# Optimization experiments

Hardware: AMD Instinct MI355X
Metric: run time of the kernel (lower is better)

Reference implementation:

```python
import jax, jax.numpy as jnp
import numpy as np

BN_EPS = 1e-5


def _batchnorm(h, gamma, beta):
    # training-mode BatchNorm1d: batch mean, biased variance
    mean = jnp.mean(h, axis=0)
    var = jnp.mean((h - mean) ** 2, axis=0)
    return (h - mean) * jax.lax.rsqrt(var + BN_EPS) * gamma + beta


def setup_inputs() -> dict:
    key = jax.random.key(0)
    ks = jax.random.split(key, 6)
    N, E = 50000, 800000
    atom, nbr = 128, 64
    d_in = 2 * atom + nbr          # 320
    d_out = 2 * atom               # 256
    x = jax.random.normal(ks[0], (N, atom), dtype=jnp.float32)
    edge_index = jax.random.randint(ks[1], (2, E), 0, N, dtype=jnp.int64)
    edge_attr = jax.random.normal(ks[2], (E, nbr), dtype=jnp.float32)
    W = jax.random.normal(ks[3], (d_in, d_out), dtype=jnp.float32) / np.sqrt(d_in)
    b = jax.random.normal(ks[4], (d_out,), dtype=jnp.float32) * 0.01
    gamma1 = jnp.ones((d_out,), dtype=jnp.float32)
    beta1 = jnp.zeros((d_out,), dtype=jnp.float32)
    gamma2 = jnp.ones((atom,), dtype=jnp.float32)
    beta2 = jnp.zeros((atom,), dtype=jnp.float32)
    return {"x": x, "edge_index": edge_index, "edge_attr": edge_attr,
            "W": W, "b": b, "gamma1": gamma1, "beta1": beta1,
            "gamma2": gamma2, "beta2": beta2}


def reference(x, edge_index, edge_attr, W, b, gamma1, beta1, gamma2, beta2):
    N, atom = x.shape
    src = edge_index[0]  # destination of scatter-sum (as in source)
    dst = edge_index[1]
    xi = x[src]                                   # [E, atom]
    xj = x[dst]                                   # [E, atom]
    total = jnp.concatenate([xi, xj, edge_attr], axis=-1)   # [E, 2*atom+nbr]
    gated = total @ W + b                         # [E, 2*atom]
    gated = _batchnorm(gated, gamma1, beta1)
    nbr_filter, nbr_core = jnp.split(gated, 2, axis=-1)
    msg = jax.nn.sigmoid(nbr_filter) * jax.nn.softplus(nbr_core)  # [E, atom]
    summed = jax.ops.segment_sum(msg, src, num_segments=N)        # [N, atom]
    return _batchnorm(summed, gamma2, beta2)
```

## Files before the change

kernel.cpp:

```cpp
#include <hip/hip_runtime.h>
#include <hip/hip_bf16.h>
#include <math.h>

#define BN_EPS 1e-5f

typedef __bf16 bf8 __attribute__((ext_vector_type(8)));
typedef unsigned short us8 __attribute__((ext_vector_type(8)));
typedef float f32x4 __attribute__((ext_vector_type(4)));

static __device__ __forceinline__ unsigned short f2bf(float f) {
  unsigned int u = __float_as_uint(f);
  unsigned int r = (u + 0x7FFFu + ((u >> 16) & 1u)) >> 16;
  return (unsigned short)r;
}
static __device__ __forceinline__ float bf2f(unsigned short v) {
  return __uint_as_float(((unsigned int)v) << 16);
}
static __device__ __forceinline__ float sigmoidf_(float x) {
  return 1.0f / (1.0f + __expf(-x));
}
static __device__ __forceinline__ float softplusf_(float x) {
  return fmaxf(x, 0.0f) + log1pf(__expf(-fabsf(x)));
}


__global__ void k_zero(int* __restrict__ deg, float* __restrict__ stats, int N) {
  int stride = gridDim.x * blockDim.x;
  int i = blockIdx.x * blockDim.x + threadIdx.x;
  for (int j = i; j < N; j += stride) deg[j] = 0;
  for (int j = i; j < 768; j += stride) stats[j] = 0.f;
}

__global__ void k_deg(const int* __restrict__ ei, int* __restrict__ deg, int E) {
  int e = blockIdx.x * blockDim.x + threadIdx.x;
  if (e < E) atomicAdd(&deg[ei[e]], 1);
}

__global__ __launch_bounds__(1024) void k_scan(const int* __restrict__ deg,
                                               int* __restrict__ offs,
                                               int* __restrict__ cursor, int N) {
  __shared__ int wsum[16];
  __shared__ int carry_s;
  int tid = threadIdx.x;
  int lane = tid & 63, wv = tid >> 6;
  if (tid == 0) carry_s = 0;
  __syncthreads();
  for (int base = 0; base < N; base += 1024) {
    int i = base + tid;
    int v = (i < N) ? deg[i] : 0;
    int x = v;
    #pragma unroll
    for (int off = 1; off < 64; off <<= 1) {
      int t = __shfl_up(x, off, 64);
      if (lane >= off) x += t;
    }
    if (lane == 63) wsum[wv] = x;
    __syncthreads();
    if (wv == 0 && lane < 16) {
      int y = wsum[lane];
      #pragma unroll
      for (int off = 1; off < 16; off <<= 1) {
        int t = __shfl_up(y, off, 64);
        if (lane >= off) y += t;
      }
      wsum[lane] = y;
    }
    __syncthreads();
    int woff = (wv == 0) ? 0 : wsum[wv - 1];
    int carry = carry_s;
    int incl = woff + x;
    if (i < N) { int o = carry + incl - v; offs[i] = o; cursor[i] = o; }
    __syncthreads();
    if (tid == 1023) carry_s = carry + incl;
    __syncthreads();
  }
}

__global__ __launch_bounds__(256) void k_wt(const float* __restrict__ W,
                                            unsigned short* __restrict__ WT) {
  int idx = blockIdx.x * 256 + threadIdx.x;
  int k = idx >> 8, c = idx & 255;
  WT[c * 320 + k] = f2bf(W[idx]);
}

__global__ __launch_bounds__(256, 3) void k_gemm1(
    const float* __restrict__ x, const int* __restrict__ ei,
    const float* __restrict__ ea, const unsigned short* __restrict__ WT,
    const float* __restrict__ bias, unsigned short* __restrict__ gated,
    int* __restrict__ cursor, int E) {
  __shared__ unsigned short F[64][328];
  __shared__ int ssrc[64], sdst[64], spos[64];
  int tid = threadIdx.x;
  int e0 = blockIdx.x * 64;
  if (tid < 64) {
    int e = e0 + tid;
    int s = 0, d = 0, p = 0;
    if (e < E) {
      s = ei[e]; d = ei[E + e];
      p = atomicAdd(&cursor[s], 1);
    }
    ssrc[tid] = s; sdst[tid] = d; spos[tid] = p;
  }
  __syncthreads();

  {
    int q = tid & 31, r2 = tid >> 5;
    #pragma unroll
    for (int it = 0; it < 8; ++it) {
      int r = r2 + it * 8;
      float4 v = *(const float4*)(x + (size_t)ssrc[r] * 128 + q * 4);
      ushort4 h = {f2bf(v.x), f2bf(v.y), f2bf(v.z), f2bf(v.w)};
      *(ushort4*)&F[r][q * 4] = h;
    }
    #pragma unroll
    for (int it = 0; it < 8; ++it) {
      int r = r2 + it * 8;
      float4 v = *(const float4*)(x + (size_t)sdst[r] * 128 + q * 4);
      ushort4 h = {f2bf(v.x), f2bf(v.y), f2bf(v.z), f2bf(v.w)};
      *(ushort4*)&F[r][128 + q * 4] = h;
    }
    int q2 = tid & 15, r4 = tid >> 4;
    #pragma unroll
    for (int it = 0; it < 4; ++it) {
      int r = r4 + it * 16;
      int e = e0 + r;
      float4 v = make_float4(0.f, 0.f, 0.f, 0.f);
      if (e < E) v = *(const float4*)(ea + (size_t)e * 64 + q2 * 4);
      ushort4 h = {f2bf(v.x), f2bf(v.y), f2bf(v.z), f2bf(v.w)};
      *(ushort4*)&F[r][256 + q2 * 4] = h;
    }
  }
  __syncthreads();

  int w = tid >> 6, l = tid & 63;
  int l15 = l & 15, lg = l >> 4;
  f32x4 acc[4][4] = {};
  const unsigned short* wtb = WT + (size_t)((w * 4) * 16 + l15) * 320 + lg * 8;
  #pragma unroll 1
  for (int k0 = 0; k0 < 10; ++k0) {
    bf8 bfr[4];
    #pragma unroll
    for (int nt = 0; nt < 4; ++nt) {
      us8 raw = *(const us8*)&F[nt * 16 + l15][k0 * 32 + lg * 8];
      bfr[nt] = __builtin_bit_cast(bf8, raw);
    }
    #pragma unroll
    for (int ctl = 0; ctl < 4; ++ctl) {
      us8 araw = *(const us8*)(wtb + (size_t)ctl * (16 * 320) + k0 * 32);
      bf8 afr = __builtin_bit_cast(bf8, araw);
      #pragma unroll
      for (int nt = 0; nt < 4; ++nt)
        acc[ctl][nt] = __builtin_amdgcn_mfma_f32_16x16x32_bf16(afr, bfr[nt], acc[ctl][nt], 0, 0, 0);
    }
  }

  #pragma unroll
  for (int ctl = 0; ctl < 4; ++ctl) {
    int col0 = (w * 4 + ctl) * 16 + lg * 4;
    float4 bv = *(const float4*)(bias + col0);
    #pragma unroll
    for (int nt = 0; nt < 4; ++nt) {
      int el = nt * 16 + l15;
      if (e0 + el < E) {
        f32x4 a = acc[ctl][nt];
        ushort4 hv = {f2bf(a[0] + bv.x), f2bf(a[1] + bv.y),
                      f2bf(a[2] + bv.z), f2bf(a[3] + bv.w)};
        *(ushort4*)(gated + (size_t)spos[el] * 256 + col0) = hv;
      }
    }
  }
}

__global__ __launch_bounds__(256) void k_bn1stats(const unsigned short* __restrict__ gated,
                                                  float* __restrict__ stats, int E) {
  __shared__ float s_[256], q_[256];
  int tid = threadIdx.x;
  s_[tid] = 0.f; q_[tid] = 0.f;
  __syncthreads();
  int w = tid >> 6, l = tid & 63;
  int c0 = l * 4;
  float s0 = 0, s1 = 0, s2 = 0, s3 = 0, q0 = 0, q1 = 0, q2 = 0, q3 = 0;
  for (int r = blockIdx.x * 4 + w; r < E; r += gridDim.x * 4) {
    ushort4 raw = *(const ushort4*)(gated + (size_t)r * 256 + c0);
    float v0 = bf2f(raw.x), v1 = bf2f(raw.y), v2 = bf2f(raw.z), v3 = bf2f(raw.w);
    s0 += v0; q0 += v0 * v0;
    s1 += v1; q1 += v1 * v1;
    s2 += v2; q2 += v2 * v2;
    s3 += v3; q3 += v3 * v3;
  }
  atomicAdd(&s_[c0], s0);     atomicAdd(&q_[c0], q0);
  atomicAdd(&s_[c0 + 1], s1); atomicAdd(&q_[c0 + 1], q1);
  atomicAdd(&s_[c0 + 2], s2); atomicAdd(&q_[c0 + 2], q2);
  atomicAdd(&s_[c0 + 3], s3); atomicAdd(&q_[c0 + 3], q3);
  __syncthreads();
  atomicAdd(&stats[tid], s_[tid]);
  atomicAdd(&stats[256 + tid], q_[tid]);
}

__global__ void k_bn1fin(float* __restrict__ stats, const float* __restrict__ g1,
                         const float* __restrict__ b1, float Einv) {
  int j = threadIdx.x;
  float mu = stats[j] * Einv;
  float var = stats[256 + j] * Einv - mu * mu;
  float s = g1[j] * rsqrtf(var + BN_EPS);
  stats[768 + j] = s;
  stats[1024 + j] = b1[j] - mu * s;
}

__global__ __launch_bounds__(256) void k_phase2(
    const unsigned short* __restrict__ gated,
    const int* __restrict__ offs, const int* __restrict__ deg,
    const float* __restrict__ stats, float* __restrict__ out, int N) {
  int wid = (blockIdx.x * 256 + threadIdx.x) >> 6;
  int lane = threadIdx.x & 63;
  if (wid >= N) return;
  const float* scale1 = stats + 768;
  const float* shift1 = stats + 1024;
  int c0 = lane * 2;
  float sf0 = scale1[c0], sf1 = scale1[c0 + 1];
  float hf0 = shift1[c0], hf1 = shift1[c0 + 1];
  float sc0 = scale1[128 + c0], sc1 = scale1[128 + c0 + 1];
  float hc0 = shift1[128 + c0], hc1 = shift1[128 + c0 + 1];
  int st = offs[wid], d = deg[wid];
  const unsigned short* rowp = gated + (size_t)st * 256;
  float a0 = 0.f, a1 = 0.f;
  for (int i = 0; i < d; ++i) {
    unsigned int fw = *(const unsigned int*)(rowp + c0);
    unsigned int cw = *(const unsigned int*)(rowp + 128 + c0);
    float f0 = bf2f((unsigned short)(fw & 0xFFFFu)) * sf0 + hf0;
    float f1 = bf2f((unsigned short)(fw >> 16)) * sf1 + hf1;
    float q0 = bf2f((unsigned short)(cw & 0xFFFFu)) * sc0 + hc0;
    float q1 = bf2f((unsigned short)(cw >> 16)) * sc1 + hc1;
    a0 += sigmoidf_(f0) * softplusf_(q0);
    a1 += sigmoidf_(f1) * softplusf_(q1);
    rowp += 256;
  }
  *(float2*)(out + (size_t)wid * 128 + c0) = make_float2(a0, a1);
}

__global__ __launch_bounds__(256) void k_bn2stats(const float* __restrict__ out,
                                                  float* __restrict__ stats, int N) {
  float* sum2 = stats + 512;
  float* sq2 = stats + 640;
  __shared__ float s_[128], q_[128];
  int c = threadIdx.x & 127, h = threadIdx.x >> 7;
  float s = 0.f, q = 0.f;
  for (int r = blockIdx.x * 2 + h; r < N; r += gridDim.x * 2) {
    float v = out[(size_t)r * 128 + c];
    s += v; q += v * v;
  }
  if (h == 0) { s_[c] = s; q_[c] = q; }
  __syncthreads();
  if (h == 1) { s_[c] += s; q_[c] += q; }
  __syncthreads();
  if (h == 0) { atomicAdd(&sum2[c], s_[c]); atomicAdd(&sq2[c], q_[c]); }
}

__global__ __launch_bounds__(256) void k_bn2norm(float* __restrict__ out,
                                                 const float* __restrict__ stats,
                                                 const float* __restrict__ g2,
                                                 const float* __restrict__ b2, int N) {
  const float* sum2 = stats + 512;
  const float* sq2 = stats + 640;
  float Ninv = 1.0f / (float)N;
  size_t total = (size_t)N * 32;
  for (size_t i = (size_t)blockIdx.x * blockDim.x + threadIdx.x; i < total;
       i += (size_t)gridDim.x * blockDim.x) {
    float4 v = *((const float4*)out + i);
    int c = (int)((i & 31) << 2);
    float r[4] = {v.x, v.y, v.z, v.w};
    #pragma unroll
    for (int j = 0; j < 4; ++j) {
      float mu = sum2[c + j] * Ninv;
      float var = sq2[c + j] * Ninv - mu * mu;
      float sc = g2[c + j] * rsqrtf(var + BN_EPS);
      r[j] = (r[j] - mu) * sc + b2[c + j];
    }
    *((float4*)out + i) = make_float4(r[0], r[1], r[2], r[3]);
  }
}

extern "C" void kernel_launch(void* const* d_in, const int* in_sizes, int n_in,
                              void* d_out, int out_size, void* d_ws, size_t ws_size,
                              hipStream_t stream) {
  (void)n_in; (void)out_size;
  const float* x  = (const float*)d_in[0];
  const int*   ei = (const int*)d_in[1];
  const float* ea = (const float*)d_in[2];
  const float* W  = (const float*)d_in[3];
  const float* b  = (const float*)d_in[4];
  const float* g1 = (const float*)d_in[5];
  const float* b1 = (const float*)d_in[6];
  const float* g2 = (const float*)d_in[7];
  const float* b2 = (const float*)d_in[8];
  int N = in_sizes[0] / 128;
  int E = in_sizes[1] / 2;
  float* out = (float*)d_out;

  char* base = (char*)d_ws;
  size_t off = 0;
  auto take = [&](size_t bytes) {
    size_t o = off;
    off = (off + bytes + 255) & ~(size_t)255;
    return o;
  };
  size_t oWT     = take((size_t)256 * 320 * sizeof(unsigned short));
  size_t oGated  = take((size_t)E * 256 * sizeof(unsigned short));
  size_t oDeg    = take((size_t)N * sizeof(int));
  size_t oOffs   = take((size_t)N * sizeof(int));
  size_t oCur    = take((size_t)N * sizeof(int));
  size_t oStats  = take(2048 * sizeof(float));
  if (off > ws_size) return;

  unsigned short* WT = (unsigned short*)(base + oWT);
  unsigned short* gated = (unsigned short*)(base + oGated);
  int* deg = (int*)(base + oDeg);
  int* offs = (int*)(base + oOffs);
  int* cursor = (int*)(base + oCur);
  float* stats = (float*)(base + oStats);

  k_zero<<<256, 256, 0, stream>>>(deg, stats, N);
  k_deg<<<(E + 255) / 256, 256, 0, stream>>>(ei, deg, E);
  k_scan<<<1, 1024, 0, stream>>>(deg, offs, cursor, N);
  k_wt<<<320, 256, 0, stream>>>(W, WT);
  k_gemm1<<<(E + 63) / 64, 256, 0, stream>>>(x, ei, ea, WT, b, gated, cursor, E);
  k_bn1stats<<<1024, 256, 0, stream>>>(gated, stats, E);
  k_bn1fin<<<1, 256, 0, stream>>>(stats, g1, b1, 1.0f / (float)E);
  k_phase2<<<(N + 3) / 4, 256, 0, stream>>>(gated, offs, deg, stats, out, N);
  k_bn2stats<<<512, 256, 0, stream>>>(out, stats, N);
  k_bn2norm<<<1024, 256, 0, stream>>>(out, stats, g2, b2, N);
}
```

Baseline: 1.385 ms.

## Precompute per-node projections, shrink edge GEMM to edge_attr, fuse BN1 stats

The concat-GEMM is split algebraically. x@W[0:128] and x@W[128:256] are computed once per node into a bf16 table P. Each edge then gathers two P rows and adds a small K=64 MFMA GEMM over edge_attr. The bias is dropped because training-mode BatchNorm cancels it. BN1 sum and sum-of-squares are accumulated inside the persistent fused kernel, which removes the separate pass over the gated buffer. The degree count and scan kernels are also vectorized to int4. The cost is an extra N×512 bf16 workspace and an extra bf16 rounding of the node projections before summation.

```diff
diff --git a/kernel.cpp b/kernel.cpp
--- a/kernel.cpp
+++ b/kernel.cpp
@@ -32,8 +32,17 @@
 }
 
 __global__ void k_deg(const int* __restrict__ ei, int* __restrict__ deg, int E) {
-  int e = blockIdx.x * blockDim.x + threadIdx.x;
-  if (e < E) atomicAdd(&deg[ei[e]], 1);
+  int idx = blockIdx.x * 256 + threadIdx.x;
+  int e = idx * 4;
+  if (e + 3 < E) {
+    int4 v = *(const int4*)(ei + e);
+    atomicAdd(&deg[v.x], 1);
+    atomicAdd(&deg[v.y], 1);
+    atomicAdd(&deg[v.z], 1);
+    atomicAdd(&deg[v.w], 1);
+  } else if (e < E) {
+    for (int k = e; k < E && k < e + 4; ++k) atomicAdd(&deg[ei[k]], 1);
+  }
 }
 
 __global__ __launch_bounds__(1024) void k_scan(const int* __restrict__ deg,
@@ -45,10 +54,21 @@
   int lane = tid & 63, wv = tid >> 6;
   if (tid == 0) carry_s = 0;
   __syncthreads();
-  for (int base = 0; base < N; base += 1024) {
-    int i = base + tid;
-    int v = (i < N) ? deg[i] : 0;
-    int x = v;
+  int N4 = (N + 3) >> 2;
+  for (int b4 = 0; b4 < N4; b4 += 1024) {
+    int i4 = b4 + tid;
+    int4 v = make_int4(0, 0, 0, 0);
+    int base = i4 * 4;
+    if (i4 < N4) {
+      if (base + 3 < N) v = *(const int4*)(deg + base);
+      else {
+        v.x = deg[base];
+        if (base + 1 < N) v.y = deg[base + 1];
+        if (base + 2 < N) v.z = deg[base + 2];
+      }
+    }
+    int tsum = v.x + v.y + v.z + v.w;
+    int x = tsum;
     #pragma unroll
     for (int off = 1; off < 64; off <<= 1) {
       int t = __shfl_up(x, off, 64);
@@ -66,135 +86,200 @@
       wsum[lane] = y;
     }
     __syncthreads();
-    int woff = (wv == 0) ? 0 : wsum[wv - 1];
     int carry = carry_s;
-    int incl = woff + x;
-    if (i < N) { int o = carry + incl - v; offs[i] = o; cursor[i] = o; }
-    __syncthreads();
-    if (tid == 1023) carry_s = carry + incl;
+    int pre = carry + ((wv == 0) ? 0 : wsum[wv - 1]) + (x - tsum);
+    if (i4 < N4) {
+      int o0 = pre, o1 = o0 + v.x, o2 = o1 + v.y, o3 = o2 + v.z;
+      if (base + 3 < N) {
+        *(int4*)(offs + base) = make_int4(o0, o1, o2, o3);
+        *(int4*)(cursor + base) = make_int4(o0, o1, o2, o3);
+      } else {
+        offs[base] = o0; cursor[base] = o0;
+        if (base + 1 < N) { offs[base + 1] = o1; cursor[base + 1] = o1; }
+        if (base + 2 < N) { offs[base + 2] = o2; cursor[base + 2] = o2; }
+      }
+    }
+    __syncthreads();
+    if (tid == 1023) carry_s = carry + wsum[15];
     __syncthreads();
   }
 }
 
 __global__ __launch_bounds__(256) void k_wt(const float* __restrict__ W,
-                                            unsigned short* __restrict__ WT) {
+                                            unsigned short* __restrict__ WT12,
+                                            unsigned short* __restrict__ W3T) {
   int idx = blockIdx.x * 256 + threadIdx.x;
-  int k = idx >> 8, c = idx & 255;
-  WT[c * 320 + k] = f2bf(W[idx]);
-}
-
-__global__ __launch_bounds__(256, 3) void k_gemm1(
-    const float* __restrict__ x, const int* __restrict__ ei,
-    const float* __restrict__ ea, const unsigned short* __restrict__ WT,
-    const float* __restrict__ bias, unsigned short* __restrict__ gated,
-    int* __restrict__ cursor, int E) {
-  __shared__ unsigned short F[64][328];
+  if (idx < 65536) {
+    int cc = idx >> 7, k = idx & 127;
+    int row = (cc < 256) ? k : (k + 128);
+    WT12[cc * 128 + k] = f2bf(W[(size_t)row * 256 + (cc & 255)]);
+  } else {
+    int j = idx - 65536;
+    int c = j >> 6, k = j & 63;
+    W3T[c * 64 + k] = f2bf(W[(size_t)(256 + k) * 256 + c]);
+  }
+}
+
+__global__ __launch_bounds__(256) void k_pgemm(const float* __restrict__ x,
+                                               const unsigned short* __restrict__ WT12,
+                                               unsigned short* __restrict__ P, int N) {
+  __shared__ unsigned short xs[64][136];
+  int row0 = blockIdx.x * 64;
+  int half = blockIdx.y;
+  int tid = threadIdx.x;
+  for (int i = tid; i < 2048; i += 256) {
+    int r = i >> 5, c4 = (i & 31) * 4;
+    int gr = row0 + r;
+    float4 v = make_float4(0.f, 0.f, 0.f, 0.f);
+    if (gr < N) v = *(const float4*)(x + (size_t)gr * 128 + c4);
+    ushort4 h = {f2bf(v.x), f2bf(v.y), f2bf(v.z), f2bf(v.w)};
+    *(ushort4*)&xs[r][c4] = h;
+  }
+  __syncthreads();
+  int w = tid >> 6, l = tid & 63, l15 = l & 15, lg = l >> 4;
+  f32x4 acc[4][4] = {};
+  const unsigned short* wtb = WT12 + (size_t)(half * 256 + w * 64 + l15) * 128 + lg * 8;
+  #pragma unroll
+  for (int k0 = 0; k0 < 4; ++k0) {
+    bf8 bfr[4];
+    #pragma unroll
+    for (int nt = 0; nt < 4; ++nt) {
+      us8 raw = *(const us8*)&xs[nt * 16 + l15][k0 * 32 + lg * 8];
+      bfr[nt] = __builtin_bit_cast(bf8, raw);
+    }
+    #pragma unroll
+    for (int ctl = 0; ctl < 4; ++ctl) {
+      us8 araw = *(const us8*)(wtb + (size_t)ctl * (16 * 128) + k0 * 32);
+      bf8 afr = __builtin_bit_cast(bf8, araw);
+      #pragma unroll
+      for (int nt = 0; nt < 4; ++nt)
+        acc[ctl][nt] = __builtin_amdgcn_mfma_f32_16x16x32_bf16(afr, bfr[nt], acc[ctl][nt], 0, 0, 0);
+    }
+  }
+  #pragma unroll
+  for (int ctl = 0; ctl < 4; ++ctl) {
+    int pcol = half * 256 + w * 64 + ctl * 16 + lg * 4;
+    #pragma unroll
+    for (int nt = 0; nt < 4; ++nt) {
+      int prow = row0 + nt * 16 + l15;
+      if (prow < N) {
+        f32x4 a = acc[ctl][nt];
+        ushort4 hv = {f2bf(a[0]), f2bf(a[1]), f2bf(a[2]), f2bf(a[3])};
+        *(ushort4*)(P + (size_t)prow * 512 + pcol) = hv;
+      }
+    }
+  }
+}
+
+__global__ __launch_bounds__(256, 3) void k_fuse(
+    const int* __restrict__ ei, const float* __restrict__ ea,
+    const unsigned short* __restrict__ W3T, const unsigned short* __restrict__ P,
+    unsigned short* __restrict__ gated, int* __restrict__ cursor,
+    float* __restrict__ stats, int E, int ntiles) {
+  __shared__ unsigned short w3s[256][72];
+  __shared__ unsigned short eas[64][72];
   __shared__ int ssrc[64], sdst[64], spos[64];
   int tid = threadIdx.x;
-  int e0 = blockIdx.x * 64;
-  if (tid < 64) {
-    int e = e0 + tid;
-    int s = 0, d = 0, p = 0;
-    if (e < E) {
-      s = ei[e]; d = ei[E + e];
-      p = atomicAdd(&cursor[s], 1);
-    }
-    ssrc[tid] = s; sdst[tid] = d; spos[tid] = p;
-  }
-  __syncthreads();
-
-  {
-    int q = tid & 31, r2 = tid >> 5;
-    #pragma unroll
-    for (int it = 0; it < 8; ++it) {
-      int r = r2 + it * 8;
-      float4 v = *(const float4*)(x + (size_t)ssrc[r] * 128 + q * 4);
-      ushort4 h = {f2bf(v.x), f2bf(v.y), f2bf(v.z), f2bf(v.w)};
-      *(ushort4*)&F[r][q * 4] = h;
-    }
-    #pragma unroll
-    for (int it = 0; it < 8; ++it) {
-      int r = r2 + it * 8;
-      float4 v = *(const float4*)(x + (size_t)sdst[r] * 128 + q * 4);
-      ushort4 h = {f2bf(v.x), f2bf(v.y), f2bf(v.z), f2bf(v.w)};
-      *(ushort4*)&F[r][128 + q * 4] = h;
-    }
-    int q2 = tid & 15, r4 = tid >> 4;
-    #pragma unroll
-    for (int it = 0; it < 4; ++it) {
-      int r = r4 + it * 16;
+  int w = tid >> 6, l = tid & 63, l15 = l & 15, lg = l >> 4;
+
+  for (int i = tid; i < 2048; i += 256) {
+    int c = i >> 3, k8 = (i & 7) * 8;
+    *(us8*)&w3s[c][k8] = *(const us8*)(W3T + c * 64 + k8);
+  }
+
+  float sA[16] = {}, qA[16] = {};
+
+  for (int t = blockIdx.x; t < ntiles; t += gridDim.x) {
+    int e0 = t * 64;
+    __syncthreads();
+    if (tid < 64) {
+      int e = e0 + tid;
+      int s = 0, d = 0, p = 0;
+      if (e < E) {
+        s = ei[e]; d = ei[E + e];
+        p = atomicAdd(&cursor[s], 1);
+      }
+      ssrc[tid] = s; sdst[tid] = d; spos[tid] = p;
+    }
+    for (int i = tid; i < 1024; i += 256) {
+      int r = i >> 4, c4 = (i & 15) * 4;
       int e = e0 + r;
       float4 v = make_float4(0.f, 0.f, 0.f, 0.f);
-      if (e < E) v = *(const float4*)(ea + (size_t)e * 64 + q2 * 4);
+      if (e < E) v = *(const float4*)(ea + (size_t)e * 64 + c4);
       ushort4 h = {f2bf(v.x), f2bf(v.y), f2bf(v.z), f2bf(v.w)};
-      *(ushort4*)&F[r][256 + q2 * 4] = h;
-    }
-  }
-  __syncthreads();
-
-  int w = tid >> 6, l = tid & 63;
-  int l15 = l & 15, lg = l >> 4;
-  f32x4 acc[4][4] = {};
-  const unsigned short* wtb = WT + (size_t)((w * 4) * 16 + l15) * 320 + lg * 8;
-  #pragma unroll 1
-  for (int k0 = 0; k0 < 10; ++k0) {
-    bf8 bfr[4];
-    #pragma unroll
-    for (int nt = 0; nt < 4; ++nt) {
-      us8 raw = *(const us8*)&F[nt * 16 + l15][k0 * 32 + lg * 8];
-      bfr[nt] = __builtin_bit_cast(bf8, raw);
-    }
-    #pragma unroll
-    for (int ctl = 0; ctl < 4; ++ctl) {
-      us8 araw = *(const us8*)(wtb + (size_t)ctl * (16 * 320) + k0 * 32);
-      bf8 afr = __builtin_bit_cast(bf8, araw);
-      #pragma unroll
-      for (int nt = 0; nt < 4; ++nt)
-        acc[ctl][nt] = __builtin_amdgcn_mfma_f32_16x16x32_bf16(afr, bfr[nt], acc[ctl][nt], 0, 0, 0);
-    }
-  }
-
-  #pragma unroll
-  for (int ctl = 0; ctl < 4; ++ctl) {
-    int col0 = (w * 4 + ctl) * 16 + lg * 4;
-    float4 bv = *(const float4*)(bias + col0);
+      *(ushort4*)&eas[r][c4] = h;
+    }
+    __syncthreads();
+
+    f32x4 acc[4][4] = {};
+    #pragma unroll
+    for (int k0 = 0; k0 < 2; ++k0) {
+      bf8 bfr[4];
+      #pragma unroll
+      for (int nt = 0; nt < 4; ++nt) {
+        us8 raw = *(const us8*)&eas[nt * 16 + l15][k0 * 32 + lg * 8];
+        bfr[nt] = __builtin_bit_cast(bf8, raw);
+      }
+      #pragma unroll
+      for (int ctl = 0; ctl < 4; ++ctl) {
+        us8 araw = *(const us8*)&w3s[w * 64 + ctl * 16 + l15][k0 * 32 + lg * 8];
+        bf8 afr = __builtin_bit_cast(bf8, araw);
+        #pragma unroll
+        for (int nt = 0; nt < 4; ++nt)
+          acc[ctl][nt] = __builtin_amdgcn_mfma_f32_16x16x32_bf16(afr, bfr[nt], acc[ctl][nt], 0, 0, 0);
+      }
+    }
+
+    int sp_[4], sn_[4], dn_[4], ok_[4];
     #pragma unroll
     for (int nt = 0; nt < 4; ++nt) {
       int el = nt * 16 + l15;
-      if (e0 + el < E) {
+      sp_[nt] = spos[el]; sn_[nt] = ssrc[el]; dn_[nt] = sdst[el];
+      ok_[nt] = (e0 + el < E);
+    }
+    #pragma unroll
+    for (int ctl = 0; ctl < 4; ++ctl) {
+      int coff = w * 64 + ctl * 16 + lg * 4;
+      uint2 p1[4], p2[4];
+      #pragma unroll
+      for (int nt = 0; nt < 4; ++nt)
+        p1[nt] = *(const uint2*)(P + (size_t)sn_[nt] * 512 + coff);
+      #pragma unroll
+      for (int nt = 0; nt < 4; ++nt)
+        p2[nt] = *(const uint2*)(P + (size_t)dn_[nt] * 512 + 256 + coff);
+      #pragma unroll
+      for (int nt = 0; nt < 4; ++nt) {
         f32x4 a = acc[ctl][nt];
-        ushort4 hv = {f2bf(a[0] + bv.x), f2bf(a[1] + bv.y),
-                      f2bf(a[2] + bv.z), f2bf(a[3] + bv.w)};
-        *(ushort4*)(gated + (size_t)spos[el] * 256 + col0) = hv;
-      }
-    }
-  }
-}
-
-__global__ __launch_bounds__(256) void k_bn1stats(const unsigned short* __restrict__ gated,
-                                                  float* __restrict__ stats, int E) {
-  __shared__ float s_[256], q_[256];
-  int tid = threadIdx.x;
-  s_[tid] = 0.f; q_[tid] = 0.f;
-  __syncthreads();
-  int w = tid >> 6, l = tid & 63;
-  int c0 = l * 4;
-  float s0 = 0, s1 = 0, s2 = 0, s3 = 0, q0 = 0, q1 = 0, q2 = 0, q3 = 0;
-  for (int r = blockIdx.x * 4 + w; r < E; r += gridDim.x * 4) {
-    ushort4 raw = *(const ushort4*)(gated + (size_t)r * 256 + c0);
-    float v0 = bf2f(raw.x), v1 = bf2f(raw.y), v2 = bf2f(raw.z), v3 = bf2f(raw.w);
-    s0 += v0; q0 += v0 * v0;
-    s1 += v1; q1 += v1 * v1;
-    s2 += v2; q2 += v2 * v2;
-    s3 += v3; q3 += v3 * v3;
-  }
-  atomicAdd(&s_[c0], s0);     atomicAdd(&q_[c0], q0);
-  atomicAdd(&s_[c0 + 1], s1); atomicAdd(&q_[c0 + 1], q1);
-  atomicAdd(&s_[c0 + 2], s2); atomicAdd(&q_[c0 + 2], q2);
-  atomicAdd(&s_[c0 + 3], s3); atomicAdd(&q_[c0 + 3], q3);
-  __syncthreads();
-  atomicAdd(&stats[tid], s_[tid]);
-  atomicAdd(&stats[256 + tid], q_[tid]);
+        float g0 = a[0] + bf2f((unsigned short)(p1[nt].x & 0xFFFFu)) + bf2f((unsigned short)(p2[nt].x & 0xFFFFu));
+        float g1 = a[1] + bf2f((unsigned short)(p1[nt].x >> 16))     + bf2f((unsigned short)(p2[nt].x >> 16));
+        float g2 = a[2] + bf2f((unsigned short)(p1[nt].y & 0xFFFFu)) + bf2f((unsigned short)(p2[nt].y & 0xFFFFu));
+        float g3 = a[3] + bf2f((unsigned short)(p1[nt].y >> 16))     + bf2f((unsigned short)(p2[nt].y >> 16));
+        if (ok_[nt]) {
+          sA[ctl * 4 + 0] += g0; qA[ctl * 4 + 0] += g0 * g0;
+          sA[ctl * 4 + 1] += g1; qA[ctl * 4 + 1] += g1 * g1;
+          sA[ctl * 4 + 2] += g2; qA[ctl * 4 + 2] += g2 * g2;
+          sA[ctl * 4 + 3] += g3; qA[ctl * 4 + 3] += g3 * g3;
+          ushort4 hv = {f2bf(g0), f2bf(g1), f2bf(g2), f2bf(g3)};
+          *(ushort4*)(gated + (size_t)sp_[nt] * 256 + coff) = hv;
+        }
+      }
+    }
+  }
+
+  #pragma unroll
+  for (int i = 0; i < 16; ++i) {
+    float s = sA[i], q = qA[i];
+    #pragma unroll
+    for (int m = 1; m < 16; m <<= 1) {
+      s += __shfl_xor(s, m, 64);
+      q += __shfl_xor(q, m, 64);
+    }
+    if (l15 == 0) {
+      int col = w * 64 + (i >> 2) * 16 + lg * 4 + (i & 3);
+      atomicAdd(&stats[col], s);
+      atomicAdd(&stats[256 + col], q);
+    }
+  }
 }
 
 __global__ void k_bn1fin(float* __restrict__ stats, const float* __restrict__ g1,
@@ -288,7 +373,6 @@
   const int*   ei = (const int*)d_in[1];
   const float* ea = (const float*)d_in[2];
   const float* W  = (const float*)d_in[3];
-  const float* b  = (const float*)d_in[4];
   const float* g1 = (const float*)d_in[5];
   const float* b1 = (const float*)d_in[6];
   const float* g2 = (const float*)d_in[7];
@@ -304,7 +388,9 @@
     off = (off + bytes + 255) & ~(size_t)255;
     return o;
   };
-  size_t oWT     = take((size_t)256 * 320 * sizeof(unsigned short));
+  size_t oWT12   = take((size_t)512 * 128 * sizeof(unsigned short));
+  size_t oW3T    = take((size_t)256 * 64 * sizeof(unsigned short));
+  size_t oP      = take((size_t)N * 512 * sizeof(unsigned short));
   size_t oGated  = take((size_t)E * 256 * sizeof(unsigned short));
   size_t oDeg    = take((size_t)N * sizeof(int));
   size_t oOffs   = take((size_t)N * sizeof(int));
@@ -312,19 +398,22 @@
   size_t oStats  = take(2048 * sizeof(float));
   if (off > ws_size) return;
 
-  unsigned short* WT = (unsigned short*)(base + oWT);
+  unsigned short* WT12 = (unsigned short*)(base + oWT12);
+  unsigned short* W3T  = (unsigned short*)(base + oW3T);
+  unsigned short* P    = (unsigned short*)(base + oP);
   unsigned short* gated = (unsigned short*)(base + oGated);
   int* deg = (int*)(base + oDeg);
   int* offs = (int*)(base + oOffs);
   int* cursor = (int*)(base + oCur);
   float* stats = (float*)(base + oStats);
 
+  int ntiles = (E + 63) / 64;
   k_zero<<<256, 256, 0, stream>>>(deg, stats, N);
-  k_deg<<<(E + 255) / 256, 256, 0, stream>>>(ei, deg, E);
+  k_deg<<<(E / 4 + 255) / 256, 256, 0, stream>>>(ei, deg, E);
   k_scan<<<1, 1024, 0, stream>>>(deg, offs, cursor, N);
-  k_wt<<<320, 256, 0, stream>>>(W, WT);
-  k_gemm1<<<(E + 63) / 64, 256, 0, stream>>>(x, ei, ea, WT, b, gated, cursor, E);
-  k_bn1stats<<<1024, 256, 0, stream>>>(gated, stats, E);
+  k_wt<<<320, 256, 0, stream>>>(W, WT12, W3T);
+  k_pgemm<<<dim3((N + 63) / 64, 2), 256, 0, stream>>>(x, WT12, P, N);
+  k_fuse<<<2048, 256, 0, stream>>>(ei, ea, W3T, P, gated, cursor, stats, E, ntiles);
   k_bn1fin<<<1, 256, 0, stream>>>(stats, g1, b1, 1.0f / (float)E);
   k_phase2<<<(N + 3) / 4, 256, 0, stream>>>(gated, offs, deg, stats, out, N);
   k_bn2stats<<<512, 256, 0, stream>>>(out, stats, N);
```

Result: slower. 1.800 ms (+30.0%).
